# Optimization experiments

Hardware: AMD Instinct MI355X
Metric: run time of the kernel (lower is better)

## Reference

```python
import jax, jax.numpy as jnp
import numpy as np

DMODEL = 1024
NUM_HEADS = 16
HEAD_DIM = DMODEL // NUM_HEADS


def setup_inputs() -> dict:
    key = jax.random.key(0)
    k_x, k_wqkv, k_bqkv, k_wo, k_bo = jax.random.split(key, 5)
    B, T, D = 4, 2048, DMODEL
    s = 1.0 / np.sqrt(D)
    return {
        "x": jax.random.normal(k_x, (B, T, D), dtype=jnp.float32),
        "w_qkv": jax.random.uniform(k_wqkv, (D, 3 * D), dtype=jnp.float32, minval=-s, maxval=s),
        "b_qkv": jax.random.uniform(k_bqkv, (3 * D,), dtype=jnp.float32, minval=-s, maxval=s),
        "w_out": jax.random.uniform(k_wo, (D, D), dtype=jnp.float32, minval=-s, maxval=s),
        "b_out": jax.random.uniform(k_bo, (D,), dtype=jnp.float32, minval=-s, maxval=s),
    }


def reference(x, w_qkv, b_qkv, w_out, b_out):
    B, T, D = x.shape
    H, Hd = NUM_HEADS, HEAD_DIM
    qkv = x @ w_qkv + b_qkv                      # [B,T,3D]
    qkv = qkv.reshape(B, T, 3, H, Hd)
    q = jnp.transpose(qkv[:, :, 0], (0, 2, 1, 3))  # [B,H,T,Hd]
    k = jnp.transpose(qkv[:, :, 1], (0, 2, 1, 3))
    v = jnp.transpose(qkv[:, :, 2], (0, 2, 1, 3))
    scores = jnp.einsum("bhqd,bhkd->bhqk", q, k) / jnp.sqrt(jnp.float32(Hd))
    weights = jax.nn.softmax(scores, axis=-1)
    attn = jnp.einsum("bhqk,bhkd->bhqd", weights, v)  # [B,H,T,Hd]
    attn = jnp.transpose(attn, (0, 2, 1, 3)).reshape(B, T, D)
    return attn @ w_out + b_out
```

## Files before the change

### kernel.cpp

```cpp
#include <hip/hip_runtime.h>
#include <hip/hip_bf16.h>


typedef __bf16 bf16_t;
typedef __bf16 bf16x8 __attribute__((ext_vector_type(8)));
typedef float f32x4 __attribute__((ext_vector_type(4)));
typedef short short4v __attribute__((ext_vector_type(4)));

#if __has_builtin(__builtin_amdgcn_mfma_f32_16x16x16_bf16)
typedef __bf16 bf16x4 __attribute__((ext_vector_type(4)));
#define MFMA_PV(va, vb, c) __builtin_amdgcn_mfma_f32_16x16x16_bf16( \
    __builtin_bit_cast(bf16x4, (va)), __builtin_bit_cast(bf16x4, (vb)), (c), 0, 0, 0)
#else
#define MFMA_PV(va, vb, c) __builtin_amdgcn_mfma_f32_16x16x16bf16_1k((va), (vb), (c), 0, 0, 0)
#endif

#define DMODEL 1024
#define NH     16
#define HD     64
#define BATCH  4
#define SEQ    2048
#define NTOK   (BATCH * SEQ)
#define NOUT   (NTOK * DMODEL)
#define CEXP   0.1803368801111204f

__device__ __forceinline__ void async_ld16(void* lds, const void* g) {
  __builtin_amdgcn_global_load_lds(
      (const __attribute__((address_space(1))) void*)g,
      (__attribute__((address_space(3))) void*)lds, 16, 0, 0);
}

__global__ __launch_bounds__(256) void sniff_dtype(
    const uint4* __restrict__ x, int* __restrict__ flag) {
  int t = threadIdx.x;
  uint4 v = x[t];
  int nanish = 0, zc = 0;
  for (int j = 0; j < 4; ++j) {
    uint4 w = x[t + j * 256];
    unsigned u[4] = {w.x, w.y, w.z, w.w};
    for (int k = 0; k < 4; ++k) {
      unsigned lo = u[k] & 0xFFFFu, hi = u[k] >> 16;
      if ((lo & 0x7F80u) == 0x7F80u) nanish++;
      if ((hi & 0x7F80u) == 0x7F80u) nanish++;
      if (lo == 0) zc++;
      if (hi == 0) zc++;
    }
  }
  (void)v;
  __shared__ int rn[256], rz[256];
  rn[t] = nanish; rz[t] = zc;
  __syncthreads();
  for (int s = 128; s > 0; s >>= 1) {
    if (t < s) { rn[t] += rn[t + s]; rz[t] += rz[t + s]; }
    __syncthreads();
  }
  if (t == 0) flag[0] = (rn[0] > 4 || rz[0] > 2048) ? 1 : 0;
}

__global__ __launch_bounds__(256) void conv_to_bf16(
    const void* __restrict__ src, bf16_t* __restrict__ dst, int n,
    const int* __restrict__ flag) {
  int i = (blockIdx.x * 256 + threadIdx.x) * 8;
  if (i >= n) return;
  if (flag[0]) {
    const float4* s = (const float4*)((const float*)src + i);
    float4 a = s[0], b = s[1];
    bf16_t* o = dst + i;
    o[0] = (bf16_t)a.x; o[1] = (bf16_t)a.y; o[2] = (bf16_t)a.z; o[3] = (bf16_t)a.w;
    o[4] = (bf16_t)b.x; o[5] = (bf16_t)b.y; o[6] = (bf16_t)b.z; o[7] = (bf16_t)b.w;
  } else {
    *(uint4*)(dst + i) = *(const uint4*)((const bf16_t*)src + i);
  }
}

__global__ __launch_bounds__(256) void conv_biases(
    const void* __restrict__ sq, const void* __restrict__ so,
    float* __restrict__ dq, float* __restrict__ dofs,
    const int* __restrict__ flag) {
  int i = blockIdx.x * 256 + threadIdx.x;
  if (i < 3072)
    dq[i] = flag[0] ? ((const float*)sq)[i] : (float)((const bf16_t*)sq)[i];
  else {
    int j = i - 3072;
    dofs[j] = flag[0] ? ((const float*)so)[j] : (float)((const bf16_t*)so)[j];
  }
}

__global__ __launch_bounds__(256) void transpose_w(
    const void* __restrict__ in, bf16_t* __restrict__ out, int R, int C,
    const int* __restrict__ flag) {
  __shared__ bf16_t tile[32][33];
  const int tx = threadIdx.x & 31, ty = threadIdx.x >> 5;
  const int c0 = blockIdx.x * 32, r0 = blockIdx.y * 32;
  if (flag[0]) {
    for (int i = 0; i < 4; ++i) {
      int r = ty + i * 8;
      tile[r][tx] = (bf16_t)((const float*)in)[(size_t)(r0 + r) * C + c0 + tx];
    }
  } else {
    for (int i = 0; i < 4; ++i) {
      int r = ty + i * 8;
      tile[r][tx] = ((const bf16_t*)in)[(size_t)(r0 + r) * C + c0 + tx];
    }
  }
  __syncthreads();
  for (int i = 0; i < 4; ++i) {
    int r = ty + i * 8;
    out[(size_t)(c0 + r) * R + r0 + tx] = tile[tx][r];
  }
}

template <int MODE>
__global__ __launch_bounds__(256) void gemm_bt_bias(
    const bf16_t* __restrict__ A, const bf16_t* __restrict__ Bt,
    const float* __restrict__ bias, void* __restrict__ Cout,
    int M, int N, int K, const int* __restrict__ flag,
    bf16_t* __restrict__ vT) {
  __shared__ bf16_t sA[128 * 32];
  __shared__ bf16_t sB[128 * 32];
  const int t = threadIdx.x;
  const int wave = t >> 6, lane = t & 63;
  const int quad = lane >> 4, l16 = lane & 15;
  const int bM = blockIdx.y * 128, bN = blockIdx.x * 128;
  const int m0w = (wave >> 1) * 64, n0w = (wave & 1) * 64;
  const int rowS = wave * 16 + (lane >> 2);
  const int kcS = (lane & 3) * 8;

  f32x4 acc[4][4] = {};

  for (int k0 = 0; k0 < K; k0 += 32) {
    for (int r = 0; r < 2; ++r) {
      int row = r * 64 + rowS;
      async_ld16((char*)sA + r * 4096 + wave * 1024,
                 A + (size_t)(bM + row) * K + k0 + kcS);
      async_ld16((char*)sB + r * 4096 + wave * 1024,
                 Bt + (size_t)(bN + row) * K + k0 + kcS);
    }
    __syncthreads();

    bf16x8 af[4], bfr[4];
    for (int i = 0; i < 4; ++i)
      af[i] = *(const bf16x8*)&sA[(m0w + i * 16 + l16) * 32 + quad * 8];
    for (int j = 0; j < 4; ++j)
      bfr[j] = *(const bf16x8*)&sB[(n0w + j * 16 + l16) * 32 + quad * 8];
    for (int i = 0; i < 4; ++i)
      for (int j = 0; j < 4; ++j)
        acc[i][j] = __builtin_amdgcn_mfma_f32_16x16x32_bf16(af[i], bfr[j], acc[i][j], 0, 0, 0);
    __syncthreads();
  }

  const bool f32out = (MODE == 1) && flag[0];
  for (int j = 0; j < 4; ++j) {
    int col = bN + n0w + j * 16 + l16;
    float bv = bias[col];
    for (int i = 0; i < 4; ++i) {
      int row0 = bM + m0w + i * 16 + quad * 4;
      if (MODE == 2 && col >= 2048) {
        int hh = (col - 2048) >> 6, dd = (col - 2048) & 63;
        bf16_t o4[4];
        for (int r = 0; r < 4; ++r) o4[r] = (bf16_t)(acc[i][j][r] + bv);
        size_t dst = ((((size_t)(row0 >> 11) * NH + hh) * HD + dd) << 11) | (row0 & 2047);
        *(uint2*)&vT[dst] = *(uint2*)o4;
      } else {
        float scale = (MODE == 2 && col < 1024) ? CEXP : 1.0f;
        for (int r = 0; r < 4; ++r) {
          float v = (acc[i][j][r] + bv) * scale;
          if (f32out) ((float*)Cout)[(size_t)(row0 + r) * N + col] = v;
          else        ((bf16_t*)Cout)[(size_t)(row0 + r) * N + col] = (bf16_t)v;
        }
      }
    }
  }
}

__global__ __launch_bounds__(256) void attention_v8(
    const bf16_t* __restrict__ qkv, const bf16_t* __restrict__ vT,
    bf16_t* __restrict__ attn) {
  const int t = threadIdx.x;
  const int wave = t >> 6, lane = t & 63;
  const int quad = lane >> 4, l16 = lane & 15;
  const int bh = blockIdx.x, b = bh >> 4, h = bh & 15;
  const int qw = blockIdx.y * 256 + wave * 64;

  __shared__ bf16_t Kt[2][128 * 64];
  __shared__ bf16_t Vt[2][64 * 128];

  const bf16_t* qglob = qkv + (size_t)b * SEQ * 3072 + h * 64;
  const bf16_t* kglob = qglob + 1024;
  const bf16_t* vglob = vT + (size_t)bh * HD * SEQ;

  bf16x8 qf[4][2];
  for (int s = 0; s < 4; ++s) {
    const bf16_t* qrow = qglob + (size_t)(qw + s * 16 + l16) * 3072 + quad * 8;
    qf[s][0] = *(const bf16x8*)qrow;
    qf[s][1] = *(const bf16x8*)(qrow + 32);
  }

  f32x4 accO[4][4] = {};
  float lpart[4] = {0.f, 0.f, 0.f, 0.f};

  const int kRow = lane >> 3, kSlot = lane & 7;
  const int vRow = lane >> 4, vSlot = lane & 15;

  auto stageKV = [&](int buf, int kt) {
    for (int j = 0; j < 4; ++j) {
      int keyl = wave * 32 + j * 8 + kRow;
      int gc = kSlot ^ (keyl & 7);
      async_ld16((char*)Kt[buf] + (wave * 32 + j * 8) * 128,
                 kglob + (size_t)(kt + keyl) * 3072 + gc * 8);
    }
    for (int j = 0; j < 4; ++j) {
      int d = wave * 16 + j * 4 + vRow;
      int gc = vSlot ^ (d & 15);
      async_ld16((char*)Vt[buf] + (wave * 16 + j * 4) * 256,
                 vglob + (size_t)d * SEQ + kt + gc * 8);
    }
  };

  stageKV(0, 0);

  for (int ti = 0; ti < SEQ / 128; ++ti) {
    const int buf = ti & 1;
    __syncthreads();
    if (ti + 1 < SEQ / 128) stageKV(buf ^ 1, (ti + 1) * 128);

    const bf16_t* KtB = Kt[buf];
    const bf16_t* VtB = Vt[buf];

    for (int kb = 0; kb < 8; ++kb) {
      const bf16_t* kr = &KtB[(kb * 16 + l16) * 64];
      bf16x8 kf0 = *(const bf16x8*)(kr + ((quad ^ (l16 & 7)) * 8));
      bf16x8 kf1 = *(const bf16x8*)(kr + (((4 + quad) ^ (l16 & 7)) * 8));

      short4v pB[4];
      for (int s = 0; s < 4; ++s) {
        f32x4 z = {0.f, 0.f, 0.f, 0.f};
        f32x4 st = __builtin_amdgcn_mfma_f32_16x16x32_bf16(kf0, qf[s][0], z, 0, 0, 0);
        st = __builtin_amdgcn_mfma_f32_16x16x32_bf16(kf1, qf[s][1], st, 0, 0, 0);
        union { bf16_t hh[4]; short4v s4; } u;
        for (int r = 0; r < 4; ++r) {
          float p = __builtin_amdgcn_exp2f(st[r]);
          lpart[s] += p;
          u.hh[r] = (bf16_t)p;
        }
        pB[s] = u.s4;
      }

      const int chunkbase = kb * 2 + (quad >> 1);
      const int coff = (quad & 1) * 4;
      for (int db = 0; db < 4; ++db) {
        short4v vf = *(const short4v*)&VtB[(db * 16 + l16) * 128 +
                                           ((chunkbase ^ l16) * 8) + coff];
        for (int s = 0; s < 4; ++s)
          accO[s][db] = MFMA_PV(vf, pB[s], accO[s][db]);
      }
    }
  }

  for (int s = 0; s < 4; ++s) {
    float l = lpart[s];
    l += __shfl_xor(l, 16);
    l += __shfl_xor(l, 32);
    float inv = 1.f / l;
    size_t tok = (size_t)b * SEQ + qw + s * 16 + l16;
    for (int db = 0; db < 4; ++db) {
      bf16_t o4[4];
      for (int r = 0; r < 4; ++r) o4[r] = (bf16_t)(accO[s][db][r] * inv);
      *(uint2*)&attn[tok * DMODEL + h * HD + db * 16 + quad * 4] = *(uint2*)o4;
    }
  }
}

extern "C" void kernel_launch(void* const* d_in, const int* in_sizes, int n_in,
                              void* d_out, int out_size, void* d_ws, size_t ws_size,
                              hipStream_t stream) {
  const void* x     = d_in[0];
  const void* w_qkv = d_in[1];
  const void* b_qkv = d_in[2];
  const void* w_out = d_in[3];
  const void* b_out = d_in[4];

  char* ws = (char*)d_ws;
  int*    flag  = (int*)ws;
  bf16_t* wqkvT = (bf16_t*)(ws + 4096);
  bf16_t* woutT = (bf16_t*)(ws + 6295552);
  float*  bqkvf = (float*)(ws + 8392704);
  float*  boutf = (float*)(ws + 8404992);
  bf16_t* qkv   = (bf16_t*)(ws + 8409088);
  bf16_t* xb    = (bf16_t*)(ws + 58740736);
  bf16_t* attn  = xb;
  bf16_t* vTbuf = (bf16_t*)(ws + 75517952);

  sniff_dtype<<<1, 256, 0, stream>>>((const uint4*)x, flag);

  conv_to_bf16<<<NOUT / 2048, 256, 0, stream>>>(x, xb, NOUT, flag);
  conv_biases<<<16, 256, 0, stream>>>(b_qkv, b_out, bqkvf, boutf, flag);

  transpose_w<<<dim3(96, 32), 256, 0, stream>>>(w_qkv, wqkvT, 1024, 3072, flag);
  transpose_w<<<dim3(32, 32), 256, 0, stream>>>(w_out, woutT, 1024, 1024, flag);

  gemm_bt_bias<2><<<dim3(24, 64), 256, 0, stream>>>(
      xb, wqkvT, bqkvf, qkv, NTOK, 3072, 1024, flag, vTbuf);

  attention_v8<<<dim3(BATCH * NH, SEQ / 256), 256, 0, stream>>>(qkv, vTbuf, attn);

  gemm_bt_bias<1><<<dim3(8, 64), 256, 0, stream>>>(
      attn, woutT, boutf, d_out, NTOK, 1024, 1024, flag, nullptr);
}
```

Before: 311.8 us.

## Shrink attention tiles and compute softmax row sums with MFMA

The attention kernel now processes 32 queries per wave and 128 per block, streaming 64-key K/V tiles instead of 128, which doubles the grid and halves LDS use to raise occupancy. The softmax denominator is accumulated by an extra MFMA against a vector of ones, replacing per-lane scalar adds and cross-lane shuffles. The V tile swizzle is changed to match the narrower layout. In exchange, each K/V tile is reused by fewer queries, so global traffic and barriers per unit of work increase.

```diff
diff --git a/kernel.cpp b/kernel.cpp
--- a/kernel.cpp
+++ b/kernel.cpp
@@ -33,7 +33,6 @@
 __global__ __launch_bounds__(256) void sniff_dtype(
     const uint4* __restrict__ x, int* __restrict__ flag) {
   int t = threadIdx.x;
-  uint4 v = x[t];
   int nanish = 0, zc = 0;
   for (int j = 0; j < 4; ++j) {
     uint4 w = x[t + j * 256];
@@ -46,7 +45,6 @@
       if (hi == 0) zc++;
     }
   }
-  (void)v;
   __shared__ int rn[256], rz[256];
   rn[t] = nanish; rz[t] = zc;
   __syncthreads();
@@ -173,95 +171,90 @@
   }
 }
 
-__global__ __launch_bounds__(256) void attention_v8(
+__global__ __launch_bounds__(256) void attention_v9(
     const bf16_t* __restrict__ qkv, const bf16_t* __restrict__ vT,
     bf16_t* __restrict__ attn) {
   const int t = threadIdx.x;
   const int wave = t >> 6, lane = t & 63;
   const int quad = lane >> 4, l16 = lane & 15;
   const int bh = blockIdx.x, b = bh >> 4, h = bh & 15;
-  const int qw = blockIdx.y * 256 + wave * 64;
-
-  __shared__ bf16_t Kt[2][128 * 64];
-  __shared__ bf16_t Vt[2][64 * 128];
+  const int qw = blockIdx.y * 128 + wave * 32;
+
+  __shared__ bf16_t Kt[2][64 * 64];
+  __shared__ bf16_t Vt[2][64 * 64];
 
   const bf16_t* qglob = qkv + (size_t)b * SEQ * 3072 + h * 64;
   const bf16_t* kglob = qglob + 1024;
   const bf16_t* vglob = vT + (size_t)bh * HD * SEQ;
 
-  bf16x8 qf[4][2];
-  for (int s = 0; s < 4; ++s) {
+  bf16x8 qf[2][2];
+  for (int s = 0; s < 2; ++s) {
     const bf16_t* qrow = qglob + (size_t)(qw + s * 16 + l16) * 3072 + quad * 8;
     qf[s][0] = *(const bf16x8*)qrow;
     qf[s][1] = *(const bf16x8*)(qrow + 32);
   }
 
-  f32x4 accO[4][4] = {};
-  float lpart[4] = {0.f, 0.f, 0.f, 0.f};
-
-  const int kRow = lane >> 3, kSlot = lane & 7;
-  const int vRow = lane >> 4, vSlot = lane & 15;
+  f32x4 accO[2][4] = {};
+  f32x4 accL[2] = {};
+  const short4v ones = {0x3F80, 0x3F80, 0x3F80, 0x3F80};
+
+  const int sRow = lane >> 3, sSlot = lane & 7;
 
   auto stageKV = [&](int buf, int kt) {
-    for (int j = 0; j < 4; ++j) {
-      int keyl = wave * 32 + j * 8 + kRow;
-      int gc = kSlot ^ (keyl & 7);
-      async_ld16((char*)Kt[buf] + (wave * 32 + j * 8) * 128,
+    for (int j = 0; j < 2; ++j) {
+      int keyl = wave * 16 + j * 8 + sRow;
+      int gc = sSlot ^ (keyl & 7);
+      async_ld16((char*)Kt[buf] + (wave * 16 + j * 8) * 128,
                  kglob + (size_t)(kt + keyl) * 3072 + gc * 8);
     }
-    for (int j = 0; j < 4; ++j) {
-      int d = wave * 16 + j * 4 + vRow;
-      int gc = vSlot ^ (d & 15);
-      async_ld16((char*)Vt[buf] + (wave * 16 + j * 4) * 256,
+    for (int j = 0; j < 2; ++j) {
+      int d = wave * 16 + j * 8 + sRow;
+      int gc = sSlot ^ (d & 7);
+      async_ld16((char*)Vt[buf] + (wave * 16 + j * 8) * 128,
                  vglob + (size_t)d * SEQ + kt + gc * 8);
     }
   };
 
   stageKV(0, 0);
 
-  for (int ti = 0; ti < SEQ / 128; ++ti) {
+  for (int ti = 0; ti < SEQ / 64; ++ti) {
     const int buf = ti & 1;
     __syncthreads();
-    if (ti + 1 < SEQ / 128) stageKV(buf ^ 1, (ti + 1) * 128);
+    if (ti + 1 < SEQ / 64) stageKV(buf ^ 1, (ti + 1) * 64);
 
     const bf16_t* KtB = Kt[buf];
     const bf16_t* VtB = Vt[buf];
 
-    for (int kb = 0; kb < 8; ++kb) {
+    for (int kb = 0; kb < 4; ++kb) {
       const bf16_t* kr = &KtB[(kb * 16 + l16) * 64];
       bf16x8 kf0 = *(const bf16x8*)(kr + ((quad ^ (l16 & 7)) * 8));
       bf16x8 kf1 = *(const bf16x8*)(kr + (((4 + quad) ^ (l16 & 7)) * 8));
 
-      short4v pB[4];
-      for (int s = 0; s < 4; ++s) {
+      short4v pB[2];
+      for (int s = 0; s < 2; ++s) {
         f32x4 z = {0.f, 0.f, 0.f, 0.f};
         f32x4 st = __builtin_amdgcn_mfma_f32_16x16x32_bf16(kf0, qf[s][0], z, 0, 0, 0);
         st = __builtin_amdgcn_mfma_f32_16x16x32_bf16(kf1, qf[s][1], st, 0, 0, 0);
         union { bf16_t hh[4]; short4v s4; } u;
-        for (int r = 0; r < 4; ++r) {
-          float p = __builtin_amdgcn_exp2f(st[r]);
-          lpart[s] += p;
-          u.hh[r] = (bf16_t)p;
-        }
+        for (int r = 0; r < 4; ++r)
+          u.hh[r] = (bf16_t)__builtin_amdgcn_exp2f(st[r]);
         pB[s] = u.s4;
+        accL[s] = MFMA_PV(ones, pB[s], accL[s]);
       }
 
       const int chunkbase = kb * 2 + (quad >> 1);
       const int coff = (quad & 1) * 4;
       for (int db = 0; db < 4; ++db) {
-        short4v vf = *(const short4v*)&VtB[(db * 16 + l16) * 128 +
-                                           ((chunkbase ^ l16) * 8) + coff];
-        for (int s = 0; s < 4; ++s)
-          accO[s][db] = MFMA_PV(vf, pB[s], accO[s][db]);
+        int d = db * 16 + l16;
+        short4v vf = *(const short4v*)&VtB[d * 64 + ((chunkbase ^ (d & 7)) * 8) + coff];
+        accO[0][db] = MFMA_PV(vf, pB[0], accO[0][db]);
+        accO[1][db] = MFMA_PV(vf, pB[1], accO[1][db]);
       }
     }
   }
 
-  for (int s = 0; s < 4; ++s) {
-    float l = lpart[s];
-    l += __shfl_xor(l, 16);
-    l += __shfl_xor(l, 32);
-    float inv = 1.f / l;
+  for (int s = 0; s < 2; ++s) {
+    float inv = 1.f / accL[s][0];
     size_t tok = (size_t)b * SEQ + qw + s * 16 + l16;
     for (int db = 0; db < 4; ++db) {
       bf16_t o4[4];
@@ -302,7 +295,7 @@
   gemm_bt_bias<2><<<dim3(24, 64), 256, 0, stream>>>(
       xb, wqkvT, bqkvf, qkv, NTOK, 3072, 1024, flag, vTbuf);
 
-  attention_v8<<<dim3(BATCH * NH, SEQ / 256), 256, 0, stream>>>(qkv, vTbuf, attn);
+  attention_v9<<<dim3(BATCH * NH, SEQ / 128), 256, 0, stream>>>(qkv, vTbuf, attn);
 
   gemm_bt_bias<1><<<dim3(8, 64), 256, 0, stream>>>(
       attn, woutT, boutf, d_out, NTOK, 1024, 1024, flag, nullptr);
```

New measurement: 317.2 us. No clear change (+1.7%).
